# Optimization experiments

Measured on AMD Instinct MI355X. Metric: run time of the kernel, lower is better.

## Reference

```python
import jax, jax.numpy as jnp
import numpy as np


def setup_inputs() -> dict:
    key = jax.random.key(0)
    ks = jax.random.split(key, 6)
    B, S, C, D, E, EMB = 512, 512, 32, 512, 8, 32
    x = jax.random.normal(ks[0], (B, S, C), dtype=jnp.float32)
    Wp = jax.random.normal(ks[1], (C, D), dtype=jnp.float32) / np.sqrt(C)
    bp = jnp.zeros((D,), dtype=jnp.float32)
    emb = jax.random.normal(ks[2], (E, EMB), dtype=jnp.float32)
    Wg = jax.random.normal(ks[3], (D + EMB,), dtype=jnp.float32) / np.sqrt(D + EMB)
    bg = jnp.zeros((1,), dtype=jnp.float32)
    We = jax.random.normal(ks[4], (E, S, D), dtype=jnp.float32) / np.sqrt(S)
    return {"x": x, "Wp": Wp, "bp": bp, "emb": emb, "Wg": Wg, "bg": bg,
            "We": We, "k": 2}


def reference(x, Wp, bp, emb, Wg, bg, We, k):
    # x: [B, S, C]  (batch, seq_len, enc_in)
    B, S, C = x.shape
    E = We.shape[0]
    # RevIN 'subtract_median' normalization along the sequence dim
    xn = x - jnp.median(x, axis=1, keepdims=True)  # [B, S, C]
    # gating context from the last timestep, projected to d_model
    ctx = xn[:, -1, :] @ Wp + bp                    # [B, D]
    # condition gate on expert-identity embeddings: concat([ctx, emb_e])
    feat = jnp.concatenate(
        [jnp.broadcast_to(ctx[:, None, :], (B, E, ctx.shape[-1])),
         jnp.broadcast_to(emb[None, :, :], (B, E, emb.shape[-1]))],
        axis=-1)                                    # [B, E, D+EMB]
    clean_logits = feat @ Wg + bg[0]                # [B, E]
    # top-k gating (eval path: no noise), softmax over the k selected logits
    top_v, top_i = jax.lax.top_k(clean_logits, k)   # [B, k]
    top_g = jax.nn.softmax(top_v, axis=-1)          # [B, k]
    gates = jnp.zeros((B, E), dtype=x.dtype)
    gates = gates.at[jnp.arange(B)[:, None], top_i].set(top_g)  # sparse [B, E]
    # per-expert linear along seq: expert e maps [S, C] -> [D, C]
    expert_out = jnp.einsum('bsv,esd->ebdv', xn, We)  # [E, B, D, C]
    # weighted scatter-combine (equals SparseDispatcher.combine since
    # gates are zero outside the top-k set)
    combined = jnp.einsum('be,ebdv->bdv', gates, expert_out)  # [B, D, C]
    return combined
```

## Files before the change

### kernel.cpp

```cpp
#include <hip/hip_runtime.h>

typedef unsigned int u32;
typedef unsigned short u16;
typedef float f32x4 __attribute__((ext_vector_type(4)));
typedef short s16x8 __attribute__((ext_vector_type(8)));

#define Bn 512
#define Sn 512
#define Cn 32
#define Dn 512

__device__ __forceinline__ u32 f2bf(float f) {
  u32 u = __float_as_uint(f);
  return (u + 0x7FFFu + ((u >> 16) & 1u)) >> 16;
}
__device__ __forceinline__ float bfl(u32 p) { return __uint_as_float(p << 16); }
__device__ __forceinline__ float bfh(u32 p) { return __uint_as_float(p & 0xFFFF0000u); }
__device__ __forceinline__ float keyToFloat(u32 k) {
  u32 u = (k & 0x80000000u) ? (k ^ 0x80000000u) : ~k;
  return __uint_as_float(u);
}
__device__ __forceinline__ void gl2lds16(const void* g, void* l) {
  __builtin_amdgcn_global_load_lds(
      (const __attribute__((address_space(1))) u32*)g,
      (__attribute__((address_space(3))) u32*)l, 16, 0, 0);
}

__global__ void k_gates(const float* __restrict__ emb, const float* __restrict__ Wg,
                        float* __restrict__ gbuf) {
  int t = threadIdx.x;
  __shared__ float ed[8];
  if (t < 8) {
    float s = 0.f;
#pragma unroll
    for (int j = 0; j < 32; ++j) s += emb[t * 32 + j] * Wg[Dn + j];
    ed[t] = s;
  }
  __syncthreads();
  if (t == 0) {
    int i1 = 0;
#pragma unroll
    for (int e = 1; e < 8; ++e) if (ed[e] > ed[i1]) i1 = e;
    int i2 = (i1 == 0) ? 1 : 0;
#pragma unroll
    for (int e = 0; e < 8; ++e) if (e != i1 && ed[e] > ed[i2]) i2 = e;
    float a = ed[i1], b = ed[i2];
    float m = fmaxf(a, b);
    float ea = __expf(a - m), eb = __expf(b - m);
    float inv = 1.f / (ea + eb);
    gbuf[0] = ea * inv;
    gbuf[1] = eb * inv;
    ((int*)gbuf)[2] = i1;
    ((int*)gbuf)[3] = i2;
  }
}

__global__ __launch_bounds__(256) void k_wmix(const float* __restrict__ We,
                                              const float* __restrict__ gbuf,
                                              u16* __restrict__ WmT) {
  __shared__ float tile[64][65];
  int bi = blockIdx.x;
  int sb = (bi & 7) * 64, db = (bi >> 3) * 64;
  float g1 = gbuf[0], g2 = gbuf[1];
  int e1 = ((const int*)gbuf)[2], e2 = ((const int*)gbuf)[3];
  const float* W1 = We + (size_t)e1 * Sn * Dn;
  const float* W2 = We + (size_t)e2 * Sn * Dn;
  int t = threadIdx.x;
#pragma unroll
  for (int i = 0; i < 16; ++i) {
    int idx = t + i * 256;
    int sl = idx >> 6, dl = idx & 63;
    int g = (sb + sl) * Dn + db + dl;
    tile[sl][dl] = g1 * W1[g] + g2 * W2[g];
  }
  __syncthreads();
#pragma unroll
  for (int i = 0; i < 16; ++i) {
    int idx = t + i * 256;
    int dl = idx >> 6, sl = idx & 63;
    WmT[(size_t)(db + dl) * Sn + sb + sl] = (u16)f2bf(tile[sl][dl]);
  }
}

__global__ void k_colsum(const u16* __restrict__ WmT, float* __restrict__ colsum) {
  int d = blockIdx.x, l = threadIdx.x;
  const uint4* p = (const uint4*)(WmT + (size_t)d * Sn + l * 8);
  uint4 u = *p;
  float s = bfl(u.x) + bfh(u.x) + bfl(u.y) + bfh(u.y) +
            bfl(u.z) + bfh(u.z) + bfl(u.w) + bfh(u.w);
#pragma unroll
  for (int off = 32; off >= 1; off >>= 1) s += __shfl_xor(s, off, 64);
  if (l == 0) colsum[d] = s;
}

__global__ __launch_bounds__(256) void k_prep(const float* __restrict__ x,
                                              float* __restrict__ med,
                                              u16* __restrict__ xbf) {
  __shared__ float buf[512][17];
  int blk = blockIdx.x;
  int b = blk >> 1, half = blk & 1;
  int vbase = half * 16;
  int t = threadIdx.x;
  int w = t >> 6, l = t & 63;
  const float4* xb4 = (const float4*)(x + (size_t)b * Sn * Cn);
  float4 f[8];
#pragma unroll
  for (int i = 0; i < 8; ++i)
    f[i] = xb4[((t >> 2) + i * 64) * 8 + half * 4 + (t & 3)];
#pragma unroll
  for (int i = 0; i < 8; ++i) {
    int s = (t >> 2) + i * 64, c0 = (t & 3) * 4;
    buf[s][c0 + 0] = f[i].x; buf[s][c0 + 1] = f[i].y;
    buf[s][c0 + 2] = f[i].z; buf[s][c0 + 3] = f[i].w;
  }
  __syncthreads();
  u32 K[4][8];
#pragma unroll
  for (int cc = 0; cc < 4; ++cc)
#pragma unroll
    for (int j = 0; j < 8; ++j) {
      u32 u = __float_as_uint(buf[j * 64 + l][w * 4 + cc]);
      K[cc][j] = (u >> 31) ? ~u : (u | 0x80000000u);
    }
  {
    int vl = t >> 4, sb = (t & 15) * 32;
    u16* orow = xbf + ((size_t)(b * 32 + vbase + vl)) * Sn;
#pragma unroll
    for (int cq = 0; cq < 4; ++cq) {
      int cp = (cq + (t & 15)) & 3;
      u32 pk[4];
#pragma unroll
      for (int jj = 0; jj < 4; ++jj) {
        u32 lo = f2bf(buf[sb + cp * 8 + jj * 2][vl]);
        u32 hi = f2bf(buf[sb + cp * 8 + jj * 2 + 1][vl]);
        pk[jj] = lo | (hi << 16);
      }
      *(uint4*)(orow + sb + cp * 8) = *(uint4*)pk;
    }
  }
  int base = b * 32 + vbase + w * 4;
#pragma unroll
  for (int cc = 0; cc < 4; ++cc) {
    u32 a1 = 0;
#pragma unroll
    for (int bit = 31; bit >= 0; --bit) {
      u32 cand = a1 | (1u << bit);
      int c = 0;
#pragma unroll
      for (int j = 0; j < 8; ++j) c += __popcll(__ballot(K[cc][j] < cand));
      if (c <= 255) a1 = cand;
    }
    int cle = 0;
#pragma unroll
    for (int j = 0; j < 8; ++j) cle += __popcll(__ballot(K[cc][j] <= a1));
    u32 a2;
    if (cle >= 257) {
      a2 = a1;
    } else {
      u32 mn = 0xFFFFFFFFu;
#pragma unroll
      for (int j = 0; j < 8; ++j) {
        u32 k2 = K[cc][j];
        if (k2 > a1 && k2 < mn) mn = k2;
      }
      mn = min(mn, (u32)__shfl_xor((int)mn, 1, 64));
      mn = min(mn, (u32)__shfl_xor((int)mn, 2, 64));
      mn = min(mn, (u32)__shfl_xor((int)mn, 4, 64));
      mn = min(mn, (u32)__shfl_xor((int)mn, 8, 64));
      mn = min(mn, (u32)__shfl_xor((int)mn, 16, 64));
      mn = min(mn, (u32)__shfl_xor((int)mn, 32, 64));
      a2 = mn;
    }
    if (l == 0) med[base + cc] = 0.5f * (keyToFloat(a1) + keyToFloat(a2));
  }
}

__global__ __launch_bounds__(256) void k_gemm(const u16* __restrict__ WmT,
                                              const u16* __restrict__ xbf,
                                              const float* __restrict__ med,
                                              const float* __restrict__ colsum,
                                              float* __restrict__ out) {
  __shared__ __align__(16) u16 As[128 * 64];
  __shared__ __align__(16) u16 Bs[128 * 64];
  int bi = blockIdx.x;
  int mb = bi & 3, nb = bi >> 2;
  int t = threadIdx.x, w = t >> 6, l = t & 63;
  int mh = (w & 1) * 64, nh = (w >> 1) * 64;
  int lane16 = l & 15, q = l >> 4;
  f32x4 acc[4][4] = {};
  int r0 = t >> 3, c = t & 7;
  const u16* Ab = WmT + (size_t)(mb * 128) * Sn;
  const u16* Bb = xbf + (size_t)(nb * 128) * Sn;
#pragma unroll 1
  for (int ch = 0; ch < 8; ++ch) {
    int k0 = ch * 64;
#pragma unroll
    for (int i = 0; i < 4; ++i) {
      int r = r0 + i * 32;
      int gc = c ^ (r & 7);
      gl2lds16(Ab + (size_t)r * Sn + k0 + gc * 8, (char*)As + t * 16 + i * 4096);
      gl2lds16(Bb + (size_t)r * Sn + k0 + gc * 8, (char*)Bs + t * 16 + i * 4096);
    }
    __syncthreads();
#pragma unroll
    for (int kk = 0; kk < 2; ++kk) {
      s16x8 af[4], bf[4];
#pragma unroll
      for (int mt = 0; mt < 4; ++mt) {
        int m = mh + mt * 16 + lane16;
        int cs = (kk * 4 + q) ^ (m & 7);
        af[mt] = *(const s16x8*)(As + m * 64 + cs * 8);
      }
#pragma unroll
      for (int nt = 0; nt < 4; ++nt) {
        int n = nh + nt * 16 + lane16;
        int cs = (kk * 4 + q) ^ (n & 7);
        bf[nt] = *(const s16x8*)(Bs + n * 64 + cs * 8);
      }
#pragma unroll
      for (int mt = 0; mt < 4; ++mt)
#pragma unroll
        for (int nt = 0; nt < 4; ++nt)
          acc[mt][nt] = __builtin_amdgcn_mfma_f32_16x16x32_bf16(af[mt], bf[nt], acc[mt][nt], 0, 0, 0);
    }
    __syncthreads();
  }
#pragma unroll
  for (int nt = 0; nt < 4; ++nt) {
    int n = nb * 128 + nh + nt * 16 + lane16;
    int b = n >> 5, v = n & 31;
    float mv = med[n];
    float* obase = out + (size_t)b * (Dn * Cn) + v;
#pragma unroll
    for (int mt = 0; mt < 4; ++mt) {
      int d0 = mb * 128 + mh + mt * 16 + q * 4;
      f32x4 cs = *(const f32x4*)(colsum + d0);
#pragma unroll
      for (int r = 0; r < 4; ++r)
        obase[(size_t)(d0 + r) * Cn] = acc[mt][nt][r] - mv * cs[r];
    }
  }
}

extern "C" void kernel_launch(void* const* d_in, const int* in_sizes, int n_in,
                              void* d_out, int out_size, void* d_ws, size_t ws_size,
                              hipStream_t stream) {
  const float* x   = (const float*)d_in[0];
  const float* emb = (const float*)d_in[3];
  const float* Wg  = (const float*)d_in[4];
  const float* We  = (const float*)d_in[6];
  float* out = (float*)d_out;
  char* ws = (char*)d_ws;
  float* gbuf   = (float*)(ws);
  float* colsum = (float*)(ws + 256);
  float* med    = (float*)(ws + 4096);
  u16*   WmT    = (u16*)(ws + 4096 + 65536);
  u16*   xbf    = (u16*)(ws + 4096 + 65536 + 524288);

  hipLaunchKernelGGL(k_gates,  dim3(1),    dim3(64),  0, stream, emb, Wg, gbuf);
  hipLaunchKernelGGL(k_wmix,   dim3(64),   dim3(256), 0, stream, We, gbuf, WmT);
  hipLaunchKernelGGL(k_colsum, dim3(512),  dim3(64),  0, stream, WmT, colsum);
  hipLaunchKernelGGL(k_prep,   dim3(1024), dim3(256), 0, stream, x, med, xbf);
  hipLaunchKernelGGL(k_gemm,   dim3(512),  dim3(256), 0, stream, WmT, xbf, med, colsum, out);
}
```

Before: 148.4 us.

## Merge gating, weight mixing, colsum and prep into one kernel

Combines the gate selection, expert-weight mixing/transposition and input median/bf16 prep into a single heterogeneous launch, with each mixing block recomputing the top-2 gates locally. Column sums become per-block partials written by the mixing blocks and reduced in the GEMM prologue through shared memory. This cuts the launch count from five to two and removes the serialization between the small gate, mix and colsum kernels. In exchange, the gate logic is computed redundantly per block and the GEMM does a small extra reduction.

```diff
diff --git a/kernel.cpp b/kernel.cpp
--- a/kernel.cpp
+++ b/kernel.cpp
@@ -14,8 +14,7 @@
   u32 u = __float_as_uint(f);
   return (u + 0x7FFFu + ((u >> 16) & 1u)) >> 16;
 }
-__device__ __forceinline__ float bfl(u32 p) { return __uint_as_float(p << 16); }
-__device__ __forceinline__ float bfh(u32 p) { return __uint_as_float(p & 0xFFFF0000u); }
+__device__ __forceinline__ float bfval(u32 bits) { return __uint_as_float(bits << 16); }
 __device__ __forceinline__ float keyToFloat(u32 k) {
   u32 u = (k & 0x80000000u) ? (k ^ 0x80000000u) : ~k;
   return __uint_as_float(u);
@@ -26,167 +25,165 @@
       (__attribute__((address_space(3))) u32*)l, 16, 0, 0);
 }
 
-__global__ void k_gates(const float* __restrict__ emb, const float* __restrict__ Wg,
-                        float* __restrict__ gbuf) {
+__global__ __launch_bounds__(256) void k_pw(const float* __restrict__ x,
+                                            const float* __restrict__ emb,
+                                            const float* __restrict__ Wg,
+                                            const float* __restrict__ We,
+                                            float* __restrict__ med,
+                                            u16* __restrict__ xbf,
+                                            u16* __restrict__ WmT,
+                                            float* __restrict__ cpart) {
+  __shared__ float buf[512][17];
+  __shared__ float ed[8];
+  int blk = blockIdx.x;
   int t = threadIdx.x;
-  __shared__ float ed[8];
-  if (t < 8) {
-    float s = 0.f;
-#pragma unroll
-    for (int j = 0; j < 32; ++j) s += emb[t * 32 + j] * Wg[Dn + j];
-    ed[t] = s;
-  }
-  __syncthreads();
-  if (t == 0) {
+
+  if (blk < 1024) {
+    int b = blk >> 1, half = blk & 1;
+    int vbase = half * 16;
+    int w = t >> 6, l = t & 63;
+    const float4* xb4 = (const float4*)(x + (size_t)b * Sn * Cn);
+    float4 f[8];
+#pragma unroll
+    for (int i = 0; i < 8; ++i)
+      f[i] = xb4[((t >> 2) + i * 64) * 8 + half * 4 + (t & 3)];
+#pragma unroll
+    for (int i = 0; i < 8; ++i) {
+      int s = (t >> 2) + i * 64, c0 = (t & 3) * 4;
+      buf[s][c0 + 0] = f[i].x; buf[s][c0 + 1] = f[i].y;
+      buf[s][c0 + 2] = f[i].z; buf[s][c0 + 3] = f[i].w;
+    }
+    __syncthreads();
+    u32 K[4][8];
+#pragma unroll
+    for (int cc = 0; cc < 4; ++cc)
+#pragma unroll
+      for (int j = 0; j < 8; ++j) {
+        u32 u = __float_as_uint(buf[j * 64 + l][w * 4 + cc]);
+        K[cc][j] = (u >> 31) ? ~u : (u | 0x80000000u);
+      }
+    {
+      int vl = t >> 4, sb = (t & 15) * 32;
+      u16* orow = xbf + ((size_t)(b * 32 + vbase + vl)) * Sn;
+#pragma unroll
+      for (int cq = 0; cq < 4; ++cq) {
+        int cp = (cq + (t & 15)) & 3;
+        u32 pk[4];
+#pragma unroll
+        for (int jj = 0; jj < 4; ++jj) {
+          u32 lo = f2bf(buf[sb + cp * 8 + jj * 2][vl]);
+          u32 hi = f2bf(buf[sb + cp * 8 + jj * 2 + 1][vl]);
+          pk[jj] = lo | (hi << 16);
+        }
+        *(uint4*)(orow + sb + cp * 8) = *(uint4*)pk;
+      }
+    }
+    int base = b * 32 + vbase + w * 4;
+#pragma unroll
+    for (int cc = 0; cc < 4; ++cc) {
+      u32 a1 = 0;
+#pragma unroll
+      for (int bit = 31; bit >= 0; --bit) {
+        u32 cand = a1 | (1u << bit);
+        int c = 0;
+#pragma unroll
+        for (int j = 0; j < 8; ++j) c += __popcll(__ballot(K[cc][j] < cand));
+        if (c <= 255) a1 = cand;
+      }
+      int cle = 0;
+#pragma unroll
+      for (int j = 0; j < 8; ++j) cle += __popcll(__ballot(K[cc][j] <= a1));
+      u32 a2;
+      if (cle >= 257) {
+        a2 = a1;
+      } else {
+        u32 mn = 0xFFFFFFFFu;
+#pragma unroll
+        for (int j = 0; j < 8; ++j) {
+          u32 k2 = K[cc][j];
+          if (k2 > a1 && k2 < mn) mn = k2;
+        }
+        mn = min(mn, (u32)__shfl_xor((int)mn, 1, 64));
+        mn = min(mn, (u32)__shfl_xor((int)mn, 2, 64));
+        mn = min(mn, (u32)__shfl_xor((int)mn, 4, 64));
+        mn = min(mn, (u32)__shfl_xor((int)mn, 8, 64));
+        mn = min(mn, (u32)__shfl_xor((int)mn, 16, 64));
+        mn = min(mn, (u32)__shfl_xor((int)mn, 32, 64));
+        a2 = mn;
+      }
+      if (l == 0) med[base + cc] = 0.5f * (keyToFloat(a1) + keyToFloat(a2));
+    }
+  } else {
+    float (*tile)[65] = (float(*)[65])&buf[0][0];
+    int bi2 = blk - 1024;
+    int si = bi2 & 7, sb = si * 64, db = (bi2 >> 3) * 64;
+    if (t < 8) {
+      float s = 0.f;
+#pragma unroll
+      for (int j = 0; j < 32; ++j) s += emb[t * 32 + j] * Wg[Dn + j];
+      ed[t] = s;
+    }
+    __syncthreads();
     int i1 = 0;
 #pragma unroll
     for (int e = 1; e < 8; ++e) if (ed[e] > ed[i1]) i1 = e;
     int i2 = (i1 == 0) ? 1 : 0;
 #pragma unroll
     for (int e = 0; e < 8; ++e) if (e != i1 && ed[e] > ed[i2]) i2 = e;
-    float a = ed[i1], b = ed[i2];
-    float m = fmaxf(a, b);
-    float ea = __expf(a - m), eb = __expf(b - m);
+    float aa = ed[i1], bb = ed[i2];
+    float m = fmaxf(aa, bb);
+    float ea = __expf(aa - m), eb = __expf(bb - m);
     float inv = 1.f / (ea + eb);
-    gbuf[0] = ea * inv;
-    gbuf[1] = eb * inv;
-    ((int*)gbuf)[2] = i1;
-    ((int*)gbuf)[3] = i2;
-  }
-}
-
-__global__ __launch_bounds__(256) void k_wmix(const float* __restrict__ We,
-                                              const float* __restrict__ gbuf,
-                                              u16* __restrict__ WmT) {
-  __shared__ float tile[64][65];
-  int bi = blockIdx.x;
-  int sb = (bi & 7) * 64, db = (bi >> 3) * 64;
-  float g1 = gbuf[0], g2 = gbuf[1];
-  int e1 = ((const int*)gbuf)[2], e2 = ((const int*)gbuf)[3];
-  const float* W1 = We + (size_t)e1 * Sn * Dn;
-  const float* W2 = We + (size_t)e2 * Sn * Dn;
-  int t = threadIdx.x;
-#pragma unroll
-  for (int i = 0; i < 16; ++i) {
-    int idx = t + i * 256;
-    int sl = idx >> 6, dl = idx & 63;
-    int g = (sb + sl) * Dn + db + dl;
-    tile[sl][dl] = g1 * W1[g] + g2 * W2[g];
-  }
-  __syncthreads();
-#pragma unroll
-  for (int i = 0; i < 16; ++i) {
-    int idx = t + i * 256;
-    int dl = idx >> 6, sl = idx & 63;
-    WmT[(size_t)(db + dl) * Sn + sb + sl] = (u16)f2bf(tile[sl][dl]);
-  }
-}
-
-__global__ void k_colsum(const u16* __restrict__ WmT, float* __restrict__ colsum) {
-  int d = blockIdx.x, l = threadIdx.x;
-  const uint4* p = (const uint4*)(WmT + (size_t)d * Sn + l * 8);
-  uint4 u = *p;
-  float s = bfl(u.x) + bfh(u.x) + bfl(u.y) + bfh(u.y) +
-            bfl(u.z) + bfh(u.z) + bfl(u.w) + bfh(u.w);
-#pragma unroll
-  for (int off = 32; off >= 1; off >>= 1) s += __shfl_xor(s, off, 64);
-  if (l == 0) colsum[d] = s;
-}
-
-__global__ __launch_bounds__(256) void k_prep(const float* __restrict__ x,
-                                              float* __restrict__ med,
-                                              u16* __restrict__ xbf) {
-  __shared__ float buf[512][17];
-  int blk = blockIdx.x;
-  int b = blk >> 1, half = blk & 1;
-  int vbase = half * 16;
-  int t = threadIdx.x;
-  int w = t >> 6, l = t & 63;
-  const float4* xb4 = (const float4*)(x + (size_t)b * Sn * Cn);
-  float4 f[8];
-#pragma unroll
-  for (int i = 0; i < 8; ++i)
-    f[i] = xb4[((t >> 2) + i * 64) * 8 + half * 4 + (t & 3)];
-#pragma unroll
-  for (int i = 0; i < 8; ++i) {
-    int s = (t >> 2) + i * 64, c0 = (t & 3) * 4;
-    buf[s][c0 + 0] = f[i].x; buf[s][c0 + 1] = f[i].y;
-    buf[s][c0 + 2] = f[i].z; buf[s][c0 + 3] = f[i].w;
-  }
-  __syncthreads();
-  u32 K[4][8];
-#pragma unroll
-  for (int cc = 0; cc < 4; ++cc)
-#pragma unroll
-    for (int j = 0; j < 8; ++j) {
-      u32 u = __float_as_uint(buf[j * 64 + l][w * 4 + cc]);
-      K[cc][j] = (u >> 31) ? ~u : (u | 0x80000000u);
-    }
-  {
-    int vl = t >> 4, sb = (t & 15) * 32;
-    u16* orow = xbf + ((size_t)(b * 32 + vbase + vl)) * Sn;
-#pragma unroll
-    for (int cq = 0; cq < 4; ++cq) {
-      int cp = (cq + (t & 15)) & 3;
-      u32 pk[4];
-#pragma unroll
-      for (int jj = 0; jj < 4; ++jj) {
-        u32 lo = f2bf(buf[sb + cp * 8 + jj * 2][vl]);
-        u32 hi = f2bf(buf[sb + cp * 8 + jj * 2 + 1][vl]);
-        pk[jj] = lo | (hi << 16);
-      }
-      *(uint4*)(orow + sb + cp * 8) = *(uint4*)pk;
-    }
-  }
-  int base = b * 32 + vbase + w * 4;
-#pragma unroll
-  for (int cc = 0; cc < 4; ++cc) {
-    u32 a1 = 0;
-#pragma unroll
-    for (int bit = 31; bit >= 0; --bit) {
-      u32 cand = a1 | (1u << bit);
-      int c = 0;
-#pragma unroll
-      for (int j = 0; j < 8; ++j) c += __popcll(__ballot(K[cc][j] < cand));
-      if (c <= 255) a1 = cand;
-    }
-    int cle = 0;
-#pragma unroll
-    for (int j = 0; j < 8; ++j) cle += __popcll(__ballot(K[cc][j] <= a1));
-    u32 a2;
-    if (cle >= 257) {
-      a2 = a1;
-    } else {
-      u32 mn = 0xFFFFFFFFu;
-#pragma unroll
-      for (int j = 0; j < 8; ++j) {
-        u32 k2 = K[cc][j];
-        if (k2 > a1 && k2 < mn) mn = k2;
-      }
-      mn = min(mn, (u32)__shfl_xor((int)mn, 1, 64));
-      mn = min(mn, (u32)__shfl_xor((int)mn, 2, 64));
-      mn = min(mn, (u32)__shfl_xor((int)mn, 4, 64));
-      mn = min(mn, (u32)__shfl_xor((int)mn, 8, 64));
-      mn = min(mn, (u32)__shfl_xor((int)mn, 16, 64));
-      mn = min(mn, (u32)__shfl_xor((int)mn, 32, 64));
-      a2 = mn;
-    }
-    if (l == 0) med[base + cc] = 0.5f * (keyToFloat(a1) + keyToFloat(a2));
+    float g1 = ea * inv, g2 = eb * inv;
+    const float* W1 = We + (size_t)i1 * Sn * Dn;
+    const float* W2 = We + (size_t)i2 * Sn * Dn;
+#pragma unroll
+    for (int i = 0; i < 16; ++i) {
+      int idx = t + i * 256;
+      int sl = idx >> 6, dl = idx & 63;
+      int g = (sb + sl) * Dn + db + dl;
+      tile[sl][dl] = g1 * W1[g] + g2 * W2[g];
+    }
+    __syncthreads();
+#pragma unroll
+    for (int i = 0; i < 16; ++i) {
+      int idx = t + i * 256;
+      int dl = idx >> 6, sl = idx & 63;
+      WmT[(size_t)(db + dl) * Sn + sb + sl] = (u16)f2bf(tile[sl][dl]);
+    }
+    {
+      int dl = t >> 2, part = t & 3;
+      float s = 0.f;
+#pragma unroll
+      for (int j = 0; j < 16; ++j)
+        s += bfval(f2bf(tile[part * 16 + j][dl]));
+      s += __shfl_xor(s, 1, 64);
+      s += __shfl_xor(s, 2, 64);
+      if (part == 0) cpart[si * 512 + db + dl] = s;
+    }
   }
 }
 
 __global__ __launch_bounds__(256) void k_gemm(const u16* __restrict__ WmT,
                                               const u16* __restrict__ xbf,
                                               const float* __restrict__ med,
-                                              const float* __restrict__ colsum,
+                                              const float* __restrict__ cpart,
                                               float* __restrict__ out) {
   __shared__ __align__(16) u16 As[128 * 64];
   __shared__ __align__(16) u16 Bs[128 * 64];
+  __shared__ float csum[512];
   int bi = blockIdx.x;
   int mb = bi & 3, nb = bi >> 2;
   int t = threadIdx.x, w = t >> 6, l = t & 63;
   int mh = (w & 1) * 64, nh = (w >> 1) * 64;
   int lane16 = l & 15, q = l >> 4;
+#pragma unroll
+  for (int d = t; d < 512; d += 256) {
+    float s = 0.f;
+#pragma unroll
+    for (int j = 0; j < 8; ++j) s += cpart[j * 512 + d];
+    csum[d] = s;
+  }
   f32x4 acc[4][4] = {};
   int r0 = t >> 3, c = t & 7;
   const u16* Ab = WmT + (size_t)(mb * 128) * Sn;
@@ -234,10 +231,9 @@
 #pragma unroll
     for (int mt = 0; mt < 4; ++mt) {
       int d0 = mb * 128 + mh + mt * 16 + q * 4;
-      f32x4 cs = *(const f32x4*)(colsum + d0);
 #pragma unroll
       for (int r = 0; r < 4; ++r)
-        obase[(size_t)(d0 + r) * Cn] = acc[mt][nt][r] - mv * cs[r];
+        obase[(size_t)(d0 + r) * Cn] = acc[mt][nt][r] - mv * csum[d0 + r];
     }
   }
 }
@@ -251,15 +247,13 @@
   const float* We  = (const float*)d_in[6];
   float* out = (float*)d_out;
   char* ws = (char*)d_ws;
-  float* gbuf   = (float*)(ws);
-  float* colsum = (float*)(ws + 256);
-  float* med    = (float*)(ws + 4096);
-  u16*   WmT    = (u16*)(ws + 4096 + 65536);
-  u16*   xbf    = (u16*)(ws + 4096 + 65536 + 524288);
-
-  hipLaunchKernelGGL(k_gates,  dim3(1),    dim3(64),  0, stream, emb, Wg, gbuf);
-  hipLaunchKernelGGL(k_wmix,   dim3(64),   dim3(256), 0, stream, We, gbuf, WmT);
-  hipLaunchKernelGGL(k_colsum, dim3(512),  dim3(64),  0, stream, WmT, colsum);
-  hipLaunchKernelGGL(k_prep,   dim3(1024), dim3(256), 0, stream, x, med, xbf);
-  hipLaunchKernelGGL(k_gemm,   dim3(512),  dim3(256), 0, stream, WmT, xbf, med, colsum, out);
-}
+  float* med   = (float*)(ws);
+  float* cpart = (float*)(ws + 65536);
+  u16*   WmT   = (u16*)(ws + 65536 + 16384);
+  u16*   xbf   = (u16*)(ws + 65536 + 16384 + 524288);
+
+  hipLaunchKernelGGL(k_pw,   dim3(1088), dim3(256), 0, stream,
+                     x, emb, Wg, We, med, xbf, WmT, cpart);
+  hipLaunchKernelGGL(k_gemm, dim3(512),  dim3(256), 0, stream,
+                     WmT, xbf, med, cpart, out);
+}
```

After: 141.2 us, median of 2. 1.05x faster.
